# Performance work log

Measured on AMD Instinct MI355X. Metric: run time of the kernel, lower is better.

Reference implementation:

```python
import jax, jax.numpy as jnp
import numpy as np

EPS = 1e-6

def setup_inputs() -> dict:
    key = jax.random.key(0)
    k1, k2 = jax.random.split(key)
    bs, n, d = 8, 4096, 3
    x = jax.random.normal(k1, (bs, n, d), dtype=jnp.float32)
    y = jax.random.normal(k2, (bs, n, d), dtype=jnp.float32)
    return {"x": x, "y": y}

def reference(x, y):
    # dist[b, i, j] = sqrt(eps + ||y[b,i] - x[b,j]||^2)  (matches x.unsqueeze(1), y.unsqueeze(2))
    x2 = jnp.sum(x * x, axis=-1)              # (bs, n)
    y2 = jnp.sum(y * y, axis=-1)              # (bs, n)
    xy = jnp.einsum('bic,bjc->bij', y, x)     # (bs, n, n)
    sq = y2[:, :, None] + x2[:, None, :] - 2.0 * xy
    dist = jnp.sqrt(EPS + jnp.maximum(sq, 0.0))
    min1 = jnp.min(dist, axis=1)              # nearest y for each x point, (bs, n)
    min2 = jnp.min(dist, axis=2)              # nearest x for each y point, (bs, n)
    return jnp.mean(min1, axis=-1) + jnp.mean(min2, axis=-1)  # (bs,)
```

## Files before the change

kernel.cpp:

```cpp
#include <hip/hip_runtime.h>
#include <math.h>

#define CH_EPS 1e-6f
#define CH_N   4096
#define CH_BS  8
#define CH_JC  16
#define CH_JCH (CH_N / CH_JC)
#define CH_TI  2

#define PART_IDX(dir, b, jc, i) \
    ((((size_t)(dir) * CH_BS + (b)) * CH_JC + (jc)) * CH_N + (i))

__global__ __launch_bounds__(256) void chamfer_scan_kernel(
    const float* __restrict__ x, const float* __restrict__ y,
    float* __restrict__ part, float* __restrict__ out) {
    const int tid = threadIdx.x;
    const int it  = blockIdx.x >> 4;
    const int jc  = blockIdx.x & 15;
    const int b   = blockIdx.y;
    const int dir = blockIdx.z;

    if (blockIdx.x == 0 && b == 0 && dir == 0 && tid < CH_BS) out[tid] = 0.0f;

    const float* own   = dir ? x : y;
    const float* other = dir ? y : x;

    __shared__ float4 q4s[CH_JCH];
    {
        const float* qsrc = other + ((size_t)b * CH_N + (size_t)jc * CH_JCH + tid) * 3;
        const float a = qsrc[0], c = qsrc[1], e = qsrc[2];
        q4s[tid] = make_float4(a, c, e, a * a + c * c + e * e);
    }
    __syncthreads();

    const int i0 = it * 512 + tid;
    const int i1 = i0 + 256;
    const float* op0 = own + ((size_t)b * CH_N + i0) * 3;
    const float* op1 = own + ((size_t)b * CH_N + i1) * 3;
    const float px0 = op0[0], py0 = op0[1], pz0 = op0[2];
    const float px1 = op1[0], py1 = op1[1], pz1 = op1[2];
    const float p20 = px0 * px0 + py0 * py0 + pz0 * pz0;
    const float p21 = px1 * px1 + py1 * py1 + pz1 * pz1;
    const float nx0 = -2.0f * px0, ny0 = -2.0f * py0, nz0 = -2.0f * pz0;
    const float nx1 = -2.0f * px1, ny1 = -2.0f * py1, nz1 = -2.0f * pz1;

    float m0[2], m1[2];
    m0[0] = m0[1] = m1[0] = m1[1] = 3.4e38f;

    for (int j0 = 0; j0 < CH_JCH; j0 += 4) {
        float4 qv[4];
#pragma unroll
        for (int k = 0; k < 4; ++k) qv[k] = q4s[j0 + k];

        const float e00 = fmaf(nx0, qv[0].x, fmaf(ny0, qv[0].y, fmaf(nz0, qv[0].z, qv[0].w)));
        const float e01 = fmaf(nx0, qv[1].x, fmaf(ny0, qv[1].y, fmaf(nz0, qv[1].z, qv[1].w)));
        const float e02 = fmaf(nx0, qv[2].x, fmaf(ny0, qv[2].y, fmaf(nz0, qv[2].z, qv[2].w)));
        const float e03 = fmaf(nx0, qv[3].x, fmaf(ny0, qv[3].y, fmaf(nz0, qv[3].z, qv[3].w)));
        const float e10 = fmaf(nx1, qv[0].x, fmaf(ny1, qv[0].y, fmaf(nz1, qv[0].z, qv[0].w)));
        const float e11 = fmaf(nx1, qv[1].x, fmaf(ny1, qv[1].y, fmaf(nz1, qv[1].z, qv[1].w)));
        const float e12 = fmaf(nx1, qv[2].x, fmaf(ny1, qv[2].y, fmaf(nz1, qv[2].z, qv[2].w)));
        const float e13 = fmaf(nx1, qv[3].x, fmaf(ny1, qv[3].y, fmaf(nz1, qv[3].z, qv[3].w)));

        m0[0] = fminf(fminf(m0[0], e00), e01);
        m0[1] = fminf(fminf(m0[1], e02), e03);
        m1[0] = fminf(fminf(m1[0], e10), e11);
        m1[1] = fminf(fminf(m1[1], e12), e13);
    }

    part[PART_IDX(dir, b, jc, i0)] = fminf(m0[0], m0[1]) + p20;
    part[PART_IDX(dir, b, jc, i1)] = fminf(m1[0], m1[1]) + p21;
}

__global__ __launch_bounds__(256) void chamfer_finalize_kernel(
    const float* __restrict__ part, float* __restrict__ out) {
    const int b   = blockIdx.x;
    const int sl  = blockIdx.y;
    const int tid = threadIdx.x;
    const int i   = sl * 256 + tid;

    float s = 0.0f;
#pragma unroll
    for (int dir = 0; dir < 2; ++dir) {
        const size_t base = PART_IDX(dir, b, 0, i);
        float m = part[base];
#pragma unroll
        for (int jc = 1; jc < CH_JC; ++jc)
            m = fminf(m, part[base + (size_t)jc * CH_N]);
        s += sqrtf(CH_EPS + fmaxf(m, 0.0f));
    }
    s *= (1.0f / (float)CH_N);

#pragma unroll
    for (int off = 32; off > 0; off >>= 1) s += __shfl_down(s, off, 64);

    __shared__ float wsum[4];
    if ((tid & 63) == 0) wsum[tid >> 6] = s;
    __syncthreads();
    if (tid == 0) atomicAdd(out + b, wsum[0] + wsum[1] + wsum[2] + wsum[3]);
}

extern "C" void kernel_launch(void* const* d_in, const int* in_sizes, int n_in,
                              void* d_out, int out_size, void* d_ws, size_t ws_size,
                              hipStream_t stream) {
    const float* x = (const float*)d_in[0];
    const float* y = (const float*)d_in[1];
    float* out  = (float*)d_out;
    float* part = (float*)d_ws;

    chamfer_scan_kernel<<<dim3(8 * CH_JC, CH_BS, 2), dim3(256), 0, stream>>>(x, y, part, out);

    chamfer_finalize_kernel<<<dim3(CH_BS, 16), dim3(256), 0, stream>>>(part, out);
}
```

Measured before the change: 30.99 us.

## Process two j-chunks per block, software-pipeline LDS loads, split finalize by direction

Each scan block now loops over two 256-point chunks of the other cloud instead of one. This halves the grid (1024 blocks) and halves the partial-min buffer written and read by finalize. The inner loop double-buffers the float4 shared-memory reads (A/B register sets) so LDS loads overlap the FMA/min work. Finalize gains a third grid dimension for direction and reduces only 8 partials per point, which adds more atomics but gives more parallelism. Fewer blocks may reduce occupancy or latency hiding across the GPU, and the extra barrier between chunks adds a sync.

```diff
diff --git a/kernel.cpp b/kernel.cpp
--- a/kernel.cpp
+++ b/kernel.cpp
@@ -4,19 +4,35 @@
 #define CH_EPS 1e-6f
 #define CH_N   4096
 #define CH_BS  8
-#define CH_JC  16
-#define CH_JCH (CH_N / CH_JC)
-#define CH_TI  2
+#define CH_JG  8
+#define CH_CPB 2
+#define CH_JCH 256
 
-#define PART_IDX(dir, b, jc, i) \
-    ((((size_t)(dir) * CH_BS + (b)) * CH_JC + (jc)) * CH_N + (i))
+#define PART_IDX(dir, b, jg, i) \
+    ((((size_t)(dir) * CH_BS + (b)) * CH_JG + (jg)) * CH_N + (i))
+
+#define CH_EVAL4(Q0, Q1, Q2, Q3)                                                        \
+    {                                                                                   \
+        const float e00 = fmaf(nx0, Q0.x, fmaf(ny0, Q0.y, fmaf(nz0, Q0.z, Q0.w)));      \
+        const float e01 = fmaf(nx0, Q1.x, fmaf(ny0, Q1.y, fmaf(nz0, Q1.z, Q1.w)));      \
+        const float e02 = fmaf(nx0, Q2.x, fmaf(ny0, Q2.y, fmaf(nz0, Q2.z, Q2.w)));      \
+        const float e03 = fmaf(nx0, Q3.x, fmaf(ny0, Q3.y, fmaf(nz0, Q3.z, Q3.w)));      \
+        const float e10 = fmaf(nx1, Q0.x, fmaf(ny1, Q0.y, fmaf(nz1, Q0.z, Q0.w)));      \
+        const float e11 = fmaf(nx1, Q1.x, fmaf(ny1, Q1.y, fmaf(nz1, Q1.z, Q1.w)));      \
+        const float e12 = fmaf(nx1, Q2.x, fmaf(ny1, Q2.y, fmaf(nz1, Q2.z, Q2.w)));      \
+        const float e13 = fmaf(nx1, Q3.x, fmaf(ny1, Q3.y, fmaf(nz1, Q3.z, Q3.w)));      \
+        ma0 = fminf(fminf(ma0, e00), e01);                              \
+        mb0 = fminf(fminf(mb0, e02), e03);                                              \
+        ma1 = fminf(fminf(ma1, e10), e11);                                              \
+        mb1 = fminf(fminf(mb1, e12), e13);                                              \
+    }
 
 __global__ __launch_bounds__(256) void chamfer_scan_kernel(
     const float* __restrict__ x, const float* __restrict__ y,
     float* __restrict__ part, float* __restrict__ out) {
     const int tid = threadIdx.x;
-    const int it  = blockIdx.x >> 4;
-    const int jc  = blockIdx.x & 15;
+    const int it  = blockIdx.x >> 3;
+    const int jg  = blockIdx.x & 7;
     const int b   = blockIdx.y;
     const int dir = blockIdx.z;
 
@@ -24,14 +40,6 @@
 
     const float* own   = dir ? x : y;
     const float* other = dir ? y : x;
-
-    __shared__ float4 q4s[CH_JCH];
-    {
-        const float* qsrc = other + ((size_t)b * CH_N + (size_t)jc * CH_JCH + tid) * 3;
-        const float a = qsrc[0], c = qsrc[1], e = qsrc[2];
-        q4s[tid] = make_float4(a, c, e, a * a + c * c + e * e);
-    }
-    __syncthreads();
 
     const int i0 = it * 512 + tid;
     const int i1 = i0 + 256;
@@ -44,51 +52,52 @@
     const float nx0 = -2.0f * px0, ny0 = -2.0f * py0, nz0 = -2.0f * pz0;
     const float nx1 = -2.0f * px1, ny1 = -2.0f * py1, nz1 = -2.0f * pz1;
 
-    float m0[2], m1[2];
-    m0[0] = m0[1] = m1[0] = m1[1] = 3.4e38f;
+    float ma0 = 3.4e38f, mb0 = 3.4e38f, ma1 = 3.4e38f, mb1 = 3.4e38f;
 
-    for (int j0 = 0; j0 < CH_JCH; j0 += 4) {
-        float4 qv[4];
+    __shared__ float4 q4s[CH_JCH];
+
 #pragma unroll
-        for (int k = 0; k < 4; ++k) qv[k] = q4s[j0 + k];
+    for (int c = 0; c < CH_CPB; ++c) {
+        const int jc = jg * CH_CPB + c;
+        if (c) __syncthreads();
+        {
+            const float* qsrc = other + ((size_t)b * CH_N + (size_t)jc * CH_JCH + tid) * 3;
+            const float qa = qsrc[0], qb = qsrc[1], qc = qsrc[2];
+            q4s[tid] = make_float4(qa, qb, qc, qa * qa + qb * qb + qc * qc);
+        }
+        __syncthreads();
 
-        const float e00 = fmaf(nx0, qv[0].x, fmaf(ny0, qv[0].y, fmaf(nz0, qv[0].z, qv[0].w)));
-        const float e01 = fmaf(nx0, qv[1].x, fmaf(ny0, qv[1].y, fmaf(nz0, qv[1].z, qv[1].w)));
-        const float e02 = fmaf(nx0, qv[2].x, fmaf(ny0, qv[2].y, fmaf(nz0, qv[2].z, qv[2].w)));
-        const float e03 = fmaf(nx0, qv[3].x, fmaf(ny0, qv[3].y, fmaf(nz0, qv[3].z, qv[3].w)));
-        const float e10 = fmaf(nx1, qv[0].x, fmaf(ny1, qv[0].y, fmaf(nz1, qv[0].z, qv[0].w)));
-        const float e11 = fmaf(nx1, qv[1].x, fmaf(ny1, qv[1].y, fmaf(nz1, qv[1].z, qv[1].w)));
-        const float e12 = fmaf(nx1, qv[2].x, fmaf(ny1, qv[2].y, fmaf(nz1, qv[2].z, qv[2].w)));
-        const float e13 = fmaf(nx1, qv[3].x, fmaf(ny1, qv[3].y, fmaf(nz1, qv[3].z, qv[3].w)));
-
-        m0[0] = fminf(fminf(m0[0], e00), e01);
-        m0[1] = fminf(fminf(m0[1], e02), e03);
-        m1[0] = fminf(fminf(m1[0], e10), e11);
-        m1[1] = fminf(fminf(m1[1], e12), e13);
+        float4 A0 = q4s[0], A1 = q4s[1], A2 = q4s[2], A3 = q4s[3];
+        float4 B0, B1, B2, B3;
+        for (int j0 = 0; j0 < CH_JCH - 8; j0 += 8) {
+            B0 = q4s[j0 + 4]; B1 = q4s[j0 + 5]; B2 = q4s[j0 + 6]; B3 = q4s[j0 + 7];
+            CH_EVAL4(A0, A1, A2, A3);
+            A0 = q4s[j0 + 8]; A1 = q4s[j0 + 9]; A2 = q4s[j0 + 10]; A3 = q4s[j0 + 11];
+            CH_EVAL4(B0, B1, B2, B3);
+        }
+        B0 = q4s[CH_JCH - 4]; B1 = q4s[CH_JCH - 3]; B2 = q4s[CH_JCH - 2]; B3 = q4s[CH_JCH - 1];
+        CH_EVAL4(A0, A1, A2, A3);
+        CH_EVAL4(B0, B1, B2, B3);
     }
 
-    part[PART_IDX(dir, b, jc, i0)] = fminf(m0[0], m0[1]) + p20;
-    part[PART_IDX(dir, b, jc, i1)] = fminf(m1[0], m1[1]) + p21;
+    part[PART_IDX(dir, b, jg, i0)] = fminf(ma0, mb0) + p20;
+    part[PART_IDX(dir, b, jg, i1)] = fminf(ma1, mb1) + p21;
 }
 
 __global__ __launch_bounds__(256) void chamfer_finalize_kernel(
     const float* __restrict__ part, float* __restrict__ out) {
     const int b   = blockIdx.x;
     const int sl  = blockIdx.y;
+    const int dir = blockIdx.z;
     const int tid = threadIdx.x;
     const int i   = sl * 256 + tid;
 
-    float s = 0.0f;
+    const size_t base = PART_IDX(dir, b, 0, i);
+    float m = part[base];
 #pragma unroll
-    for (int dir = 0; dir < 2; ++dir) {
-        const size_t base = PART_IDX(dir, b, 0, i);
-        float m = part[base];
-#pragma unroll
-        for (int jc = 1; jc < CH_JC; ++jc)
-            m = fminf(m, part[base + (size_t)jc * CH_N]);
-        s += sqrtf(CH_EPS + fmaxf(m, 0.0f));
-    }
-    s *= (1.0f / (float)CH_N);
+    for (int jg = 1; jg < CH_JG; ++jg)
+        m = fminf(m, part[base + (size_t)jg * CH_N]);
+    float s = sqrtf(CH_EPS + fmaxf(m, 0.0f)) * (1.0f / (float)CH_N);
 
 #pragma unroll
     for (int off = 32; off > 0; off >>= 1) s += __shfl_down(s, off, 64);
@@ -107,7 +116,7 @@
     float* out  = (float*)d_out;
     float* part = (float*)d_ws;
 
-    chamfer_scan_kernel<<<dim3(8 * CH_JC, CH_BS, 2), dim3(256), 0, stream>>>(x, y, part, out);
+    chamfer_scan_kernel<<<dim3(8 * CH_JG, CH_BS, 2), dim3(256), 0, stream>>>(x, y, part, out);
 
-    chamfer_finalize_kernel<<<dim3(CH_BS, 16), dim3(256), 0, stream>>>(part, out);
+    chamfer_finalize_kernel<<<dim3(CH_BS, 16, 2), dim3(256), 0, stream>>>(part, out);
 }
```

Measured after the change: 33.92 us. 1.09x slower.
